# Optimization experiments

Hardware: AMD Instinct MI355X
Metric: run time of the kernel (lower is better)

## Reference

```python
import jax, jax.numpy as jnp
import numpy as np

B, N, T_OBS, N_HEAD = 64, 512, 8, 4
IN_FEAT = T_OBS * 2          # 16
OUT_FEAT = IN_FEAT * 4       # 64 (GAT out / MLP in)
HID1, HID2 = 1024, 512
S, NSAMP = 2, 20
OUT_DIM = S * NSAMP          # 40


def setup_inputs() -> dict:
    key = jax.random.key(0)
    ks = jax.random.split(key, 12)
    x = jax.random.normal(ks[0], (B, N, T_OBS, 2), dtype=jnp.float32)
    # binary adjacency-style mask over the dense node-node attention
    mask = (jax.random.uniform(ks[1], (B, 1, N, N)) > 0.1).astype(jnp.float32)
    xav = lambda k, shp, fi, fo: jax.random.uniform(k, shp, jnp.float32, -1.0, 1.0) * (1.414 * np.sqrt(6.0 / (fi + fo)))
    w = xav(ks[2], (N_HEAD, IN_FEAT, OUT_FEAT), IN_FEAT, OUT_FEAT)
    a_src = xav(ks[3], (N_HEAD, OUT_FEAT, 1), OUT_FEAT, 1)
    a_dst = xav(ks[4], (N_HEAD, OUT_FEAT, 1), OUT_FEAT, 1)
    bias = jnp.zeros((OUT_FEAT,), jnp.float32)
    lin = lambda k, fi, fo: jax.random.uniform(k, (fi, fo), jnp.float32, -1.0, 1.0) * np.sqrt(1.0 / fi)
    W1 = lin(ks[5], OUT_FEAT, HID1); b1 = jnp.zeros((HID1,), jnp.float32)
    W2 = lin(ks[6], HID1, HID2);     b2 = jnp.zeros((HID2,), jnp.float32)
    W3 = lin(ks[7], HID2, OUT_DIM);  b3 = jnp.zeros((OUT_DIM,), jnp.float32)
    return {"x": x, "mask": mask, "w": w, "a_src": a_src, "a_dst": a_dst,
            "bias": bias, "W1": W1, "b1": b1, "W2": W2, "b2": b2, "W3": W3, "b3": b3}


def reference(x, mask, w, a_src, a_dst, bias, W1, b1, W2, b2, W3, b3):
    b, n = x.shape[0], x.shape[1]
    node = x.reshape(b, n, -1)                                   # [B,N,16]
    # per-head projection: [B,N,16] x [H,16,64] -> [B,H,N,64]
    h_prime = jnp.einsum('bni,hio->bhno', node, w)
    attn_src = jnp.einsum('bhno,ho->bhn', h_prime, a_src[..., 0])
    attn_dst = jnp.einsum('bhno,ho->bhn', h_prime, a_dst[..., 0])
    attn = attn_src[..., :, None] * attn_dst[..., None, :]       # [B,H,N,N] outer product
    attn = jnp.where(attn >= 0, attn, 0.2 * attn)                # leaky_relu(0.2)
    attn = jax.nn.softmax(attn, axis=-1)
    # dropout is identity in eval mode
    attn = attn * mask
    out = jnp.einsum('bhnm,bhmo->bno', attn, h_prime) + bias     # sum over heads fused
    out = out + h_prime.sum(axis=1)                              # skip connection
    # MLP: activation BEFORE each linear (as in original MLP.forward)
    y = out
    for W, bb in ((W1, b1), (W2, b2), (W3, b3)):
        y = jax.nn.relu(y) @ W + bb
    y = y.reshape(b, n, NSAMP, -1)[..., 0:S]                     # [B,N,20,2]
    return jnp.clip(jax.nn.sigmoid(y), 0.01, 0.99)
```

## Files before the change

### kernel.cpp

```cpp
#include <hip/hip_runtime.h>
#include <math.h>

typedef short bf16x8 __attribute__((ext_vector_type(8)));
typedef float f32x4 __attribute__((ext_vector_type(4)));

#define BB 64
#define NN 512
#define NH 4
#define FI 16
#define FO 64
#define HD1 1024
#define HD2 512
#define ODIM 40

__device__ __forceinline__ unsigned short f2bf(float f) {
    unsigned u = __float_as_uint(f);
    u += 0x7fffu + ((u >> 16) & 1u);
    return (unsigned short)(u >> 16);
}
__device__ __forceinline__ unsigned pack2(float a, float b) {
    return (unsigned)f2bf(a) | ((unsigned)f2bf(b) << 16);
}
__device__ __forceinline__ void gload16(const void* g, void* l) {
    __builtin_amdgcn_global_load_lds(
        (const __attribute__((address_space(1))) unsigned int*)g,
        (__attribute__((address_space(3))) unsigned int*)l,
        16, 0, 0);
}

__global__ void k_wa(const float* __restrict__ w, const float* __restrict__ a_src,
                     const float* __restrict__ a_dst, float* __restrict__ wa)
{
    int t = threadIdx.x;
    int h = t >> 4;
    float s = 0.f, d = 0.f;
    for (int o = 0; o < FO; ++o) {
        float wv = w[t*FO + o];
        s = fmaf(wv, a_src[h*FO + o], s);
        d = fmaf(wv, a_dst[h*FO + o], d);
    }
    wa[t] = s; wa[64 + t] = d;
}

__global__ __launch_bounds__(256) void k_pack(
    const float* __restrict__ mask, unsigned char* __restrict__ mbits)
{
    __shared__ unsigned char lb[4][64];
    int t = threadIdx.x;
    int r = t >> 6, l = t & 63;
    size_t R = (size_t)blockIdx.x * 4 + r;
    const float4* src = (const float4*)(mask + R*NN + l*8);
    float4 a = src[0], bq = src[1];
    unsigned byte = 0;
    byte |= (a.x  != 0.f) ? 1u   : 0u;
    byte |= (a.y  != 0.f) ? 2u   : 0u;
    byte |= (a.z  != 0.f) ? 4u   : 0u;
    byte |= (a.w  != 0.f) ? 8u   : 0u;
    byte |= (bq.x != 0.f) ? 16u  : 0u;
    byte |= (bq.y != 0.f) ? 32u  : 0u;
    byte |= (bq.z != 0.f) ? 64u  : 0u;
    byte |= (bq.w != 0.f) ? 128u : 0u;
    lb[r][(l & 3)*16 + (l >> 2)] = (unsigned char)byte;
    __syncthreads();
    if (t < 16) {
        int rr = t >> 2, seg = t & 3;
        uint4 v = *(uint4*)&lb[rr][seg*16];
        *(uint4*)&mbits[((size_t)blockIdx.x*4 + rr)*64 + seg*16] = v;
    }
}

__global__ __launch_bounds__(256) void k_proj2(
    const float* __restrict__ x, const float* __restrict__ w,
    const float* __restrict__ bias, const float* __restrict__ wa,
    short* __restrict__ hpT,
    float* __restrict__ asrc, float* __restrict__ adst,
    float* __restrict__ gat)
{
    __shared__ float xS[64][20];
    __shared__ float gS[NH][64][64];
    int b = blockIdx.y;
    int n0 = blockIdx.x * 64;
    int t = threadIdx.x;
    int h = t >> 6, o = t & 63;
    {
        int n = t >> 2, q = t & 3;
        float4 v = *(const float4*)&x[((size_t)b*NN + n0 + n)*FI + q*4];
        *(float4*)&xS[n][q*4] = v;
    }
    float wreg[16];
#pragma unroll
    for (int i = 0; i < FI; ++i) wreg[i] = w[(h*FI + i)*FO + o];
    __syncthreads();

    short* hb = hpT + (size_t)b * (NH*FO*NN);
    for (int nc = 0; nc < 8; ++nc) {
        float acc[8];
#pragma unroll
        for (int k = 0; k < 8; ++k) {
            int n = nc*8 + k;
            float4 a0 = *(const float4*)&xS[n][0];
            float4 a1 = *(const float4*)&xS[n][4];
            float4 a2 = *(const float4*)&xS[n][8];
            float4 a3 = *(const float4*)&xS[n][12];
            float sA = fmaf(a0.x, wreg[0], fmaf(a0.y, wreg[1], fmaf(a0.z, wreg[2], a0.w*wreg[3])));
            float sB = fmaf(a1.x, wreg[4], fmaf(a1.y, wreg[5], fmaf(a1.z, wreg[6], a1.w*wreg[7])));
            float sC = fmaf(a2.x, wreg[8], fmaf(a2.y, wreg[9], fmaf(a2.z, wreg[10], a2.w*wreg[11])));
            float sD = fmaf(a3.x, wreg[12], fmaf(a3.y, wreg[13], fmaf(a3.z, wreg[14], a3.w*wreg[15])));
            float s = (sA + sB) + (sC + sD);
            acc[k] = s;
            gS[h][n][o] = s;
        }
        uint4 p;
        p.x = pack2(acc[0], acc[1]); p.y = pack2(acc[2], acc[3]);
        p.z = pack2(acc[4], acc[5]); p.w = pack2(acc[6], acc[7]);
        int jt = (n0 >> 5) + (nc >> 2);
        *(uint4*)&hb[(size_t)(jt*256 + h*64 + o)*32 + (nc & 3)*8] = p;
    }
    {
        int n = o;
        float vs = 0.f, vd = 0.f;
#pragma unroll
        for (int i = 0; i < FI; ++i) {
            float xv = xS[n][i];
            vs = fmaf(xv, wa[h*FI + i], vs);
            vd = fmaf(xv, wa[64 + h*FI + i], vd);
        }
        asrc[(size_t)(b*NH + h)*NN + n0 + n] = vs;
        adst[(size_t)(b*NH + h)*NN + n0 + n] = vd;
    }
    __syncthreads();
#pragma unroll
    for (int r = 0; r < 16; ++r) {
        int idx = t + r*256;
        int n = idx >> 6, oo = idx & 63;
        float g = bias[oo] + ((gS[0][n][oo] + gS[1][n][oo]) + (gS[2][n][oo] + gS[3][n][oo]));
        gat[((size_t)b*NN + n0 + n)*FO + oo] = g;
    }
}

__global__ __launch_bounds__(512, 2) void k_attn2(
    const short* __restrict__ hpT, const unsigned char* __restrict__ mbits,
    const float* __restrict__ asrc, const float* __restrict__ adst,
    float* __restrict__ gat)
{
    __shared__ float dS[NH*NN];
    __shared__ float dmaxS[NH], dminS[NH];
    __shared__ float part[4*4*64*4];
    int b = blockIdx.y;
    int i0blk = blockIdx.x * 64;
    int t = threadIdx.x;
#pragma unroll
    for (int r = 0; r < 4; ++r) {
        int idx = t + r*512;
        dS[idx] = adst[(size_t)b*(NH*NN) + idx];
    }
    __syncthreads();
    int wave = t >> 6, lane = t & 63;
    int wv4 = wave & 3, hh = (wave >> 2) * 2;
    if (wave < 4) {
        float mx = -INFINITY, mn = INFINITY;
        const float* dh = &dS[wave*NN];
#pragma unroll
        for (int q = 0; q < 8; ++q) {
            float v = dh[lane*8 + q];
            mx = fmaxf(mx, v); mn = fminf(mn, v);
        }
#pragma unroll
        for (int off = 1; off < 64; off <<= 1) {
            mx = fmaxf(mx, __shfl_xor(mx, off));
            mn = fminf(mn, __shfl_xor(mn, off));
        }
        if (lane == 0) { dmaxS[wave] = mx; dminS[wave] = mn; }
    }
    __syncthreads();
    int li = lane & 15, kq = lane >> 4;
    int i = i0blk + wv4*16 + li;
    float s[2], m[2], Ssum[2];
#pragma unroll
    for (int h2 = 0; h2 < 2; ++h2) {
        int h = hh + h2;
        s[h2] = asrc[(size_t)(b*NH + h)*NN + i];
        float dm = s[h2] >= 0.f ? dmaxS[h] : dminS[h];
        float l = s[h2] * dm;
        m[h2] = fmaxf(l, 0.2f*l);
        Ssum[h2] = 0.f;
    }
    f32x4 accH[2][4];
#pragma unroll
    for (int h2 = 0; h2 < 2; ++h2)
#pragma unroll
        for (int ot = 0; ot < 4; ++ot) accH[h2][ot] = (f32x4)0.f;

    unsigned mwarr[4];
    {
        uint4 mv = *(const uint4*)(mbits + ((size_t)(b*NN + i))*64 + kq*16);
        mwarr[0] = mv.x; mwarr[1] = mv.y; mwarr[2] = mv.z; mwarr[3] = mv.w;
    }
    const short* vb = hpT + (size_t)b * (NH*FO*NN);
#pragma unroll
    for (int jt = 0; jt < 16; ++jt) {
        unsigned mbyte = (mwarr[jt >> 2] >> ((jt & 3) * 8)) & 0xffu;
        int j0 = jt*32;
#pragma unroll
        for (int h2 = 0; h2 < 2; ++h2) {
            int h = hh + h2;
            float4 d0 = *(const float4*)&dS[h*NN + j0 + kq*8];
            float4 d1 = *(const float4*)&dS[h*NN + j0 + kq*8 + 4];
            float dv[8] = {d0.x,d0.y,d0.z,d0.w,d1.x,d1.y,d1.z,d1.w};
            float u[8];
#pragma unroll
            for (int q = 0; q < 8; ++q) {
                float v = s[h2]*dv[q];
                v = fmaxf(v, 0.2f*v);
                u[q] = __expf(v - m[h2]);
            }
            Ssum[h2] += ((u[0]+u[1]) + (u[2]+u[3])) + ((u[4]+u[5]) + (u[6]+u[7]));
            float mu[8];
#pragma unroll
            for (int q = 0; q < 8; ++q)
                mu[q] = ((mbyte >> q) & 1u) ? u[q] : 0.f;
            union { bf16x8 v; unsigned uu[4]; } pf;
#pragma unroll
            for (int q = 0; q < 4; ++q)
                pf.uu[q] = pack2(mu[2*q], mu[2*q+1]);
            __builtin_amdgcn_s_setprio(1);
#pragma unroll
            for (int ot = 0; ot < 4; ++ot) {
                bf16x8 vf = *(const bf16x8*)&vb[(size_t)(jt*256 + h*64 + ot*16 + li)*32 + kq*8];
                accH[h2][ot] = __builtin_amdgcn_mfma_f32_16x16x32_bf16(pf.v, vf, accH[h2][ot], 0, 0, 0);
            }
            __builtin_amdgcn_s_setprio(0);
        }
    }
#pragma unroll
    for (int h2 = 0; h2 < 2; ++h2) {
        Ssum[h2] += __shfl_xor(Ssum[h2], 16);
        Ssum[h2] += __shfl_xor(Ssum[h2], 32);
    }
    float rinv[2][4];
#pragma unroll
    for (int h2 = 0; h2 < 2; ++h2)
#pragma unroll
        for (int g = 0; g < 4; ++g)
            rinv[h2][g] = 1.0f / __shfl(Ssum[h2], kq*4 + g);
    f32x4 contrib[4];
#pragma unroll
    for (int ot = 0; ot < 4; ++ot)
#pragma unroll
        for (int g = 0; g < 4; ++g)
            contrib[ot][g] = accH[0][ot][g]*rinv[0][g] + accH[1][ot][g]*rinv[1][g];
    if (wave < 4) {
#pragma unroll
        for (int ot = 0; ot < 4; ++ot) {
            float4 v = {contrib[ot][0], contrib[ot][1], contrib[ot][2], contrib[ot][3]};
            *(float4*)&part[((wv4*4 + ot)*64 + lane)*4] = v;
        }
    }
    __syncthreads();
    if (wave >= 4) {
#pragma unroll
        for (int ot = 0; ot < 4; ++ot) {
            float4 p = *(const float4*)&part[((wv4*4 + ot)*64 + lane)*4];
#pragma unroll
            for (int g = 0; g < 4; ++g) {
                int ii = i0blk + wv4*16 + kq*4 + g;
                int oo = ot*16 + li;
                size_t ix = ((size_t)b*NN + ii)*FO + oo;
                float pg = (g == 0) ? p.x : (g == 1) ? p.y : (g == 2) ? p.z : p.w;
                gat[ix] += contrib[ot][g] + pg;
            }
        }
    }
}

__global__ __launch_bounds__(256) void k_conv(
    const float* __restrict__ W1, const float* __restrict__ W2, const float* __restrict__ W3,
    short* __restrict__ w1t, short* __restrict__ w2f, short* __restrict__ w3t)
{
    int idx = blockIdx.x * 256 + threadIdx.x;
    if (idx < HD1*FO) {
        int n = idx >> 6, k = idx & 63;
        w1t[idx] = (short)f2bf(W1[k*HD1 + n]);
    } else if (idx < HD1*FO + HD2*HD1) {
        int i2 = idx - HD1*FO;
        int e = i2 & 7, kqq = (i2 >> 3) & 3, n = (i2 >> 5) & 511, ks = i2 >> 14;
        int k = ks*32 + kqq*8 + e;
        w2f[i2] = (short)f2bf(W2[k*HD2 + n]);
    } else if (idx < HD1*FO + HD2*HD1 + 48*HD2) {
        int i3 = idx - (HD1*FO + HD2*HD1);
        int n = i3 >> 9, k = i3 & 511;
        w3t[i3] = (short)(n < ODIM ? f2bf(W3[k*ODIM + n]) : 0);
    }
}

__global__ __launch_bounds__(256, 2) void k_mlpA(
    const float* __restrict__ gat,
    const short* __restrict__ w1t, const float* __restrict__ b1,
    short* __restrict__ h1g)
{
    __shared__ char a0b[8192];
    int t = threadIdx.x;
    int lane = t & 63, wave = t >> 6;
    int li = lane & 15, kq = lane >> 4;
    int m0 = blockIdx.x * 64;

    {
        int row = t >> 2, c0 = (t & 3) * 16;
        const float4* g = (const float4*)&gat[(size_t)(m0 + row) * FO + c0];
        float4 v0 = g[0], v1 = g[1], v2 = g[2], v3 = g[3];
        uint4 p0, p1;
        p0.x = pack2(fmaxf(v0.x,0.f), fmaxf(v0.y,0.f));
        p0.y = pack2(fmaxf(v0.z,0.f), fmaxf(v0.w,0.f));
        p0.z = pack2(fmaxf(v1.x,0.f), fmaxf(v1.y,0.f));
        p0.w = pack2(fmaxf(v1.z,0.f), fmaxf(v1.w,0.f));
        p1.x = pack2(fmaxf(v2.x,0.f), fmaxf(v2.y,0.f));
        p1.y = pack2(fmaxf(v2.z,0.f), fmaxf(v2.w,0.f));
        p1.z = pack2(fmaxf(v3.x,0.f), fmaxf(v3.y,0.f));
        p1.w = pack2(fmaxf(v3.z,0.f), fmaxf(v3.w,0.f));
        int base = row*128 + c0*2;
        *(uint4*)(a0b + (base ^ ((row&7)<<4)))      = p0;
        *(uint4*)(a0b + ((base+16) ^ ((row&7)<<4))) = p1;
    }
    __syncthreads();

    for (int c = 0; c < 4; ++c) {
        int n0 = wave * 256 + c * 64;
        f32x4 acc[4][4];
#pragma unroll
        for (int mt = 0; mt < 4; ++mt)
#pragma unroll
            for (int nt = 0; nt < 4; ++nt) acc[mt][nt] = (f32x4)0.f;
#pragma unroll
        for (int ks = 0; ks < 2; ++ks) {
            int k0 = ks * 32;
            bf16x8 xf[4];
#pragma unroll
            for (int mt = 0; mt < 4; ++mt) {
                int row = mt * 16 + li;
                int addr = (row * 128 + k0 * 2 + kq * 16) ^ ((row & 7) << 4);
                xf[mt] = *(bf16x8*)(a0b + addr);
            }
#pragma unroll
            for (int nt = 0; nt < 4; ++nt) {
                int col = n0 + nt * 16 + li;
                bf16x8 wf = *(const bf16x8*)(w1t + col * 64 + k0 + kq * 8);
#pragma unroll
                for (int mt = 0; mt < 4; ++mt)
                    acc[mt][nt] = __builtin_amdgcn_mfma_f32_16x16x32_bf16(wf, xf[mt], acc[mt][nt], 0, 0, 0);
            }
        }
#pragma unroll
        for (int mt = 0; mt < 4; ++mt)
#pragma unroll
            for (int nt = 0; nt < 4; ++nt) {
                int m = mt * 16 + li;
                int nb = n0 + nt * 16 + kq * 4;
                float4 bb = *(const float4*)&b1[nb];
                float v0 = fmaxf(acc[mt][nt][0] + bb.x, 0.f);
                float v1 = fmaxf(acc[mt][nt][1] + bb.y, 0.f);
                float v2 = fmaxf(acc[mt][nt][2] + bb.z, 0.f);
                float v3 = fmaxf(acc[mt][nt][3] + bb.w, 0.f);
                uint2 pw; pw.x = pack2(v0, v1); pw.y = pack2(v2, v3);
                *(uint2*)&h1g[(size_t)(m0 + m) * HD1 + nb] = pw;
            }
    }
}

__global__ __launch_bounds__(512, 2) void k_mlpB(
    const short* __restrict__ h1g,
    const short* __restrict__ w2f, const float* __restrict__ b2,
    const short* __restrict__ w3t, const float* __restrict__ b3,
    float* __restrict__ out)
{
    extern __shared__ char smem[];
    int t = threadIdx.x;
    int lane = t & 63, wave = t >> 6;
    int li = lane & 15, kq = lane >> 4;
    int m0 = blockIdx.x * 128;

    auto STAGE = [&](int i, int ks) {
        char* base = smem + i * 8192;
        int row = wave * 16 + (lane >> 2);
        int slotS = (lane & 3) ^ ((row >> 1) & 3);
        const short* src = h1g + (size_t)(m0 + row) * HD1 + ks * 32 + slotS * 8;
        gload16(src, base + wave * 1024);
    };
    const short* wfbase = w2f + ((size_t)(wave*64 + li)*4 + kq)*8;

    f32x4 acc2[8][4];
#pragma unroll
    for (int mt = 0; mt < 8; ++mt)
#pragma unroll
        for (int nt = 0; nt < 4; ++nt) acc2[mt][nt] = (f32x4)0.f;

    bf16x8 wf0[4], wf1[4];
    __builtin_amdgcn_sched_barrier(0);
    STAGE(0, 0);
#pragma unroll
    for (int nt = 0; nt < 4; ++nt) wf0[nt] = *(const bf16x8*)(wfbase + 0*16384 + nt*512);
    __builtin_amdgcn_sched_barrier(0);
    STAGE(1, 1);
#pragma unroll
    for (int nt = 0; nt < 4; ++nt) wf1[nt] = *(const bf16x8*)(wfbase + 1*16384 + nt*512);
    __builtin_amdgcn_sched_barrier(0);

    for (int ks = 0; ks < 32; ++ks) {
        int cur = ks & 1;
        if (ks < 31) { asm volatile("s_waitcnt vmcnt(5)" ::: "memory"); }
        else         { asm volatile("s_waitcnt vmcnt(0)" ::: "memory"); }
        __builtin_amdgcn_sched_barrier(0);
        __builtin_amdgcn_s_barrier();
        __builtin_amdgcn_sched_barrier(0);

        char* base = smem + cur * 8192;
        bf16x8 xf[8];
#pragma unroll
        for (int mt = 0; mt < 8; ++mt) {
            int m = mt * 16 + li;
            int slot = kq ^ ((m >> 1) & 3);
            xf[mt] = *(bf16x8*)(base + m * 64 + slot * 16);
        }
        asm volatile("s_waitcnt lgkmcnt(0)" ::: "memory");
        __builtin_amdgcn_sched_barrier(0);
        __builtin_amdgcn_s_barrier();
        __builtin_amdgcn_sched_barrier(0);

        bf16x8 wfn[4];
        if (ks < 30) {
            STAGE(cur, ks + 2);
#pragma unroll
            for (int nt = 0; nt < 4; ++nt)
                wfn[nt] = *(const bf16x8*)(wfbase + (size_t)(ks+2)*16384 + nt*512);
        }
        __builtin_amdgcn_sched_barrier(0);

        __builtin_amdgcn_s_setprio(1);
#pragma unroll
        for (int nt = 0; nt < 4; ++nt)
#pragma unroll
            for (int mt = 0; mt < 8; ++mt)
                acc2[mt][nt] = __builtin_amdgcn_mfma_f32_16x16x32_bf16(wf0[nt], xf[mt], acc2[mt][nt], 0, 0, 0);
        __builtin_amdgcn_s_setprio(0);
        if (ks < 30) {
#pragma unroll
            for (int nt = 0; nt < 4; ++nt) { wf0[nt] = wf1[nt]; wf1[nt] = wfn[nt]; }
        } else {
#pragma unroll
            for (int nt = 0; nt < 4; ++nt) wf0[nt] = wf1[nt];
        }
    }
    __syncthreads();

#pragma unroll
    for (int mt = 0; mt < 8; ++mt)
#pragma unroll
        for (int nt = 0; nt < 4; ++nt) {
            int m = mt * 16 + li;
            int nb = wave * 64 + nt * 16 + kq * 4;
            float4 bb = *(const float4*)&b2[nb];
            float v0 = fmaxf(acc2[mt][nt][0] + bb.x, 0.f);
            float v1 = fmaxf(acc2[mt][nt][1] + bb.y, 0.f);
            float v2 = fmaxf(acc2[mt][nt][2] + bb.z, 0.f);
            float v3 = fmaxf(acc2[mt][nt][3] + bb.w, 0.f);
            uint2 pw; pw.x = pack2(v0, v1); pw.y = pack2(v2, v3);
            int addr = (m * 1024 + nb * 2) ^ ((m & 7) << 4);
            *(uint2*)(smem + addr) = pw;
        }
    __syncthreads();

    f32x4 acc3[3];
#pragma unroll
    for (int nt = 0; nt < 3; ++nt) acc3[nt] = (f32x4)0.f;
#pragma unroll
    for (int ks = 0; ks < 16; ++ks) {
        int k0 = ks * 32;
        int m = wave * 16 + li;
        int addr = (m * 1024 + k0 * 2 + kq * 16) ^ ((m & 7) << 4);
        bf16x8 xfr = *(bf16x8*)(smem + addr);
#pragma unroll
        for (int nt = 0; nt < 3; ++nt) {
            int col = nt * 16 + li;
            bf16x8 wfr = *(const bf16x8*)(w3t + col * 512 + k0 + kq * 8);
            acc3[nt] = __builtin_amdgcn_mfma_f32_16x16x32_bf16(wfr, xfr, acc3[nt], 0, 0, 0);
        }
    }
#pragma unroll
    for (int nt = 0; nt < 3; ++nt)
#pragma unroll
        for (int g = 0; g < 4; ++g) {
            int n = nt * 16 + kq * 4 + g;
            if (n < ODIM) {
                int m = wave * 16 + li;
                float s = acc3[nt][g] + b3[n];
                s = 1.f / (1.f + __expf(-s));
                s = fminf(fmaxf(s, 0.01f), 0.99f);
                out[(size_t)(m0 + m) * ODIM + n] = s;
            }
        }
}

extern "C" void kernel_launch(void* const* d_in, const int* in_sizes, int n_in,
                              void* d_out, int out_size, void* d_ws, size_t ws_size,
                              hipStream_t stream)
{
    const float* x     = (const float*)d_in[0];
    const float* mask  = (const float*)d_in[1];
    const float* w     = (const float*)d_in[2];
    const float* a_src = (const float*)d_in[3];
    const float* a_dst = (const float*)d_in[4];
    const float* bias  = (const float*)d_in[5];
    const float* W1    = (const float*)d_in[6];
    const float* b1    = (const float*)d_in[7];
    const float* W2    = (const float*)d_in[8];
    const float* b2    = (const float*)d_in[9];
    const float* W3    = (const float*)d_in[10];
    const float* b3    = (const float*)d_in[11];
    float* out = (float*)d_out;

    char* p = (char*)d_ws;
    short* h1g = (short*)p;
    short* hpT = (short*)p;  p += (size_t)BB*NH*FO*NN*2;
    float* asrc = (float*)p; p += (size_t)BB*NH*NN*4;
    float* adst = (float*)p; p += (size_t)BB*NH*NN*4;
    p = (char*)d_ws + (size_t)BB*NN*HD1*2;
    float* gat  = (float*)p; p += (size_t)BB*NN*FO*4;
    short* w1t  = (short*)p; p += (size_t)HD1*FO*2;
    short* w2f  = (short*)p; p += (size_t)HD2*HD1*2;
    short* w3t  = (short*)p; p += (size_t)48*HD2*2;
    float* wa   = (float*)p; p += 128*4;
    unsigned char* mbits = (unsigned char*)p; p += (size_t)BB*NN*64;

    k_wa   <<<1, 64, 0, stream>>>(w, a_src, a_dst, wa);
    k_pack <<<BB*NN/4, 256, 0, stream>>>(mask, mbits);
    k_conv <<<(HD1*FO + HD2*HD1 + 48*HD2)/256, 256, 0, stream>>>(W1, W2, W3, w1t, w2f, w3t);
    k_proj2<<<dim3(NN/64, BB), 256, 0, stream>>>(x, w, bias, wa, hpT, asrc, adst, gat);
    k_attn2<<<dim3(NN/64, BB), 512, 0, stream>>>(hpT, mbits, asrc, adst, gat);
    k_mlpA <<<BB*NN/64, 256, 0, stream>>>(gat, w1t, b1, h1g);
    k_mlpB <<<BB*NN/128, 512, 131072, stream>>>(h1g, w2f, b2, w3t, b3, out);
}
```

Baseline: 160.4 us.

## Fuse first MLP layer into second-layer kernel, producing h1 tiles in LDS

Measured after the change: 156.9 us. -2.2%, faster.

```diff
diff --git a/kernel.cpp b/kernel.cpp
--- a/kernel.cpp
+++ b/kernel.cpp
@@ -20,12 +20,6 @@
 }
 __device__ __forceinline__ unsigned pack2(float a, float b) {
     return (unsigned)f2bf(a) | ((unsigned)f2bf(b) << 16);
-}
-__device__ __forceinline__ void gload16(const void* g, void* l) {
-    __builtin_amdgcn_global_load_lds(
-        (const __attribute__((address_space(1))) unsigned int*)g,
-        (__attribute__((address_space(3))) unsigned int*)l,
-        16, 0, 0);
 }
 
 __global__ void k_wa(const float* __restrict__ w, const float* __restrict__ a_src,
@@ -293,16 +287,20 @@
     }
 }
 
-__global__ __launch_bounds__(256, 2) void k_mlpA(
+__global__ __launch_bounds__(512, 2) void k_mlpB(
     const float* __restrict__ gat,
     const short* __restrict__ w1t, const float* __restrict__ b1,
-    short* __restrict__ h1g)
-{
-    __shared__ char a0b[8192];
+    const short* __restrict__ w2f, const float* __restrict__ b2,
+    const short* __restrict__ w3t, const float* __restrict__ b3,
+    float* __restrict__ out)
+{
+    extern __shared__ char smem[];
+    char* a0b = smem;
+    char* h1s = smem + 16384;
     int t = threadIdx.x;
     int lane = t & 63, wave = t >> 6;
     int li = lane & 15, kq = lane >> 4;
-    int m0 = blockIdx.x * 64;
+    int m0 = blockIdx.x * 128;
 
     {
         int row = t >> 2, c0 = (t & 3) * 16;
@@ -323,68 +321,38 @@
     }
     __syncthreads();
 
-    for (int c = 0; c < 4; ++c) {
-        int n0 = wave * 256 + c * 64;
-        f32x4 acc[4][4];
-#pragma unroll
-        for (int mt = 0; mt < 4; ++mt)
-#pragma unroll
-            for (int nt = 0; nt < 4; ++nt) acc[mt][nt] = (f32x4)0.f;
-#pragma unroll
-        for (int ks = 0; ks < 2; ++ks) {
-            int k0 = ks * 32;
-            bf16x8 xf[4];
-#pragma unroll
-            for (int mt = 0; mt < 4; ++mt) {
-                int row = mt * 16 + li;
-                int addr = (row * 128 + k0 * 2 + kq * 16) ^ ((row & 7) << 4);
-                xf[mt] = *(bf16x8*)(a0b + addr);
-            }
-#pragma unroll
-            for (int nt = 0; nt < 4; ++nt) {
-                int col = n0 + nt * 16 + li;
-                bf16x8 wf = *(const bf16x8*)(w1t + col * 64 + k0 + kq * 8);
-#pragma unroll
-                for (int mt = 0; mt < 4; ++mt)
-                    acc[mt][nt] = __builtin_amdgcn_mfma_f32_16x16x32_bf16(wf, xf[mt], acc[mt][nt], 0, 0, 0);
-            }
-        }
-#pragma unroll
-        for (int mt = 0; mt < 4; ++mt)
-#pragma unroll
-            for (int nt = 0; nt < 4; ++nt) {
-                int m = mt * 16 + li;
-                int nb = n0 + nt * 16 + kq * 4;
-                float4 bb = *(const float4*)&b1[nb];
-                float v0 = fmaxf(acc[mt][nt][0] + bb.x, 0.f);
-                float v1 = fmaxf(acc[mt][nt][1] + bb.y, 0.f);
-                float v2 = fmaxf(acc[mt][nt][2] + bb.z, 0.f);
-                float v3 = fmaxf(acc[mt][nt][3] + bb.w, 0.f);
-                uint2 pw; pw.x = pack2(v0, v1); pw.y = pack2(v2, v3);
-                *(uint2*)&h1g[(size_t)(m0 + m) * HD1 + nb] = pw;
-            }
-    }
-}
-
-__global__ __launch_bounds__(512, 2) void k_mlpB(
-    const short* __restrict__ h1g,
-    const short* __restrict__ w2f, const float* __restrict__ b2,
-    const short* __restrict__ w3t, const float* __restrict__ b3,
-    float* __restrict__ out)
-{
-    extern __shared__ char smem[];
-    int t = threadIdx.x;
-    int lane = t & 63, wave = t >> 6;
-    int li = lane & 15, kq = lane >> 4;
-    int m0 = blockIdx.x * 128;
-
-    auto STAGE = [&](int i, int ks) {
-        char* base = smem + i * 8192;
-        int row = wave * 16 + (lane >> 2);
-        int slotS = (lane & 3) ^ ((row >> 1) & 3);
-        const short* src = h1g + (size_t)(m0 + row) * HD1 + ks * 32 + slotS * 8;
-        gload16(src, base + wave * 1024);
+    bf16x8 a0f[2];
+#pragma unroll
+    for (int k0s = 0; k0s < 2; ++k0s) {
+        int row = wave*16 + li;
+        int addr = (row*128 + k0s*64 + kq*16) ^ ((row&7)<<4);
+        a0f[k0s] = *(bf16x8*)(a0b + addr);
+    }
+
+    auto PRODUCE = [&](int bufi, int ks) {
+        char* hb = h1s + bufi*8192;
+#pragma unroll
+        for (int klt = 0; klt < 2; ++klt) {
+            int n = ks*32 + klt*16 + li;
+            bf16x8 w1f0 = *(const bf16x8*)(w1t + n*64 + kq*8);
+            bf16x8 w1f1 = *(const bf16x8*)(w1t + n*64 + 32 + kq*8);
+            f32x4 ah = (f32x4)0.f;
+            ah = __builtin_amdgcn_mfma_f32_16x16x32_bf16(w1f0, a0f[0], ah, 0, 0, 0);
+            ah = __builtin_amdgcn_mfma_f32_16x16x32_bf16(w1f1, a0f[1], ah, 0, 0, 0);
+            int m = wave*16 + li;
+            int nb = ks*32 + klt*16 + kq*4;
+            float4 bb = *(const float4*)&b1[nb];
+            float v0 = fmaxf(ah[0] + bb.x, 0.f);
+            float v1 = fmaxf(ah[1] + bb.y, 0.f);
+            float v2 = fmaxf(ah[2] + bb.z, 0.f);
+            float v3 = fmaxf(ah[3] + bb.w, 0.f);
+            uint2 pw; pw.x = pack2(v0, v1); pw.y = pack2(v2, v3);
+            int s0 = klt*2 + (kq >> 1);
+            int p = s0 ^ ((m >> 1) & 3);
+            *(uint2*)(hb + m*64 + p*16 + (kq & 1)*8) = pw;
+        }
     };
+
     const short* wfbase = w2f + ((size_t)(wave*64 + li)*4 + kq)*8;
 
     f32x4 acc2[8][4];
@@ -393,61 +361,53 @@
 #pragma unroll
         for (int nt = 0; nt < 4; ++nt) acc2[mt][nt] = (f32x4)0.f;
 
-    bf16x8 wf0[4], wf1[4];
+    PRODUCE(0, 0);
+    asm volatile("s_waitcnt lgkmcnt(0)" ::: "memory");
     __builtin_amdgcn_sched_barrier(0);
-    STAGE(0, 0);
-#pragma unroll
-    for (int nt = 0; nt < 4; ++nt) wf0[nt] = *(const bf16x8*)(wfbase + 0*16384 + nt*512);
-    __builtin_amdgcn_sched_barrier(0);
-    STAGE(1, 1);
-#pragma unroll
-    for (int nt = 0; nt < 4; ++nt) wf1[nt] = *(const bf16x8*)(wfbase + 1*16384 + nt*512);
+    __builtin_amdgcn_s_barrier();
     __builtin_amdgcn_sched_barrier(0);
 
     for (int ks = 0; ks < 32; ++ks) {
         int cur = ks & 1;
-        if (ks < 31) { asm volatile("s_waitcnt vmcnt(5)" ::: "memory"); }
-        else         { asm volatile("s_waitcnt vmcnt(0)" ::: "memory"); }
+        bf16x8 wf[4];
+#pragma unroll
+        for (int nt = 0; nt < 4; ++nt)
+            wf[nt] = *(const bf16x8*)(wfbase + (size_t)ks*16384 + nt*512);
+        char* base = h1s + cur*8192;
+        bf16x8 xfa[4];
+#pragma unroll
+        for (int mt = 0; mt < 4; ++mt) {
+            int m = mt * 16 + li;
+            int slot = kq ^ ((m >> 1) & 3);
+            xfa[mt] = *(bf16x8*)(base + m * 64 + slot * 16);
+        }
+        if (ks < 31) PRODUCE(cur ^ 1, ks + 1);
+        asm volatile("s_waitcnt lgkmcnt(0)" ::: "memory");
+        __builtin_amdgcn_sched_barrier(0);
+        __builtin_amdgcn_s_setprio(1);
+#pragma unroll
+        for (int nt = 0; nt < 4; ++nt)
+#pragma unroll
+            for (int mt = 0; mt < 4; ++mt)
+                acc2[mt][nt] = __builtin_amdgcn_mfma_f32_16x16x32_bf16(wf[nt], xfa[mt], acc2[mt][nt], 0, 0, 0);
+        bf16x8 xfb[4];
+#pragma unroll
+        for (int mt = 0; mt < 4; ++mt) {
+            int m = (mt + 4) * 16 + li;
+            int slot = kq ^ ((m >> 1) & 3);
+            xfb[mt] = *(bf16x8*)(base + m * 64 + slot * 16);
+        }
+        asm volatile("s_waitcnt lgkmcnt(0)" ::: "memory");
+        __builtin_amdgcn_sched_barrier(0);
+#pragma unroll
+        for (int nt = 0; nt < 4; ++nt)
+#pragma unroll
+            for (int mt = 0; mt < 4; ++mt)
+                acc2[mt+4][nt] = __builtin_amdgcn_mfma_f32_16x16x32_bf16(wf[nt], xfb[mt], acc2[mt+4][nt], 0, 0, 0);
+        __builtin_amdgcn_s_setprio(0);
         __builtin_amdgcn_sched_barrier(0);
         __builtin_amdgcn_s_barrier();
         __builtin_amdgcn_sched_barrier(0);
-
-        char* base = smem + cur * 8192;
-        bf16x8 xf[8];
-#pragma unroll
-        for (int mt = 0; mt < 8; ++mt) {
-            int m = mt * 16 + li;
-            int slot = kq ^ ((m >> 1) & 3);
-            xf[mt] = *(bf16x8*)(base + m * 64 + slot * 16);
-        }
-        asm volatile("s_waitcnt lgkmcnt(0)" ::: "memory");
-        __builtin_amdgcn_sched_barrier(0);
-        __builtin_amdgcn_s_barrier();
-        __builtin_amdgcn_sched_barrier(0);
-
-        bf16x8 wfn[4];
-        if (ks < 30) {
-            STAGE(cur, ks + 2);
-#pragma unroll
-            for (int nt = 0; nt < 4; ++nt)
-                wfn[nt] = *(const bf16x8*)(wfbase + (size_t)(ks+2)*16384 + nt*512);
-        }
-        __builtin_amdgcn_sched_barrier(0);
-
-        __builtin_amdgcn_s_setprio(1);
-#pragma unroll
-        for (int nt = 0; nt < 4; ++nt)
-#pragma unroll
-            for (int mt = 0; mt < 8; ++mt)
-                acc2[mt][nt] = __builtin_amdgcn_mfma_f32_16x16x32_bf16(wf0[nt], xf[mt], acc2[mt][nt], 0, 0, 0);
-        __builtin_amdgcn_s_setprio(0);
-        if (ks < 30) {
-#pragma unroll
-            for (int nt = 0; nt < 4; ++nt) { wf0[nt] = wf1[nt]; wf1[nt] = wfn[nt]; }
-        } else {
-#pragma unroll
-            for (int nt = 0; nt < 4; ++nt) wf0[nt] = wf1[nt];
-        }
     }
     __syncthreads();
 
@@ -518,11 +478,9 @@
     float* out = (float*)d_out;
 
     char* p = (char*)d_ws;
-    short* h1g = (short*)p;
     short* hpT = (short*)p;  p += (size_t)BB*NH*FO*NN*2;
     float* asrc = (float*)p; p += (size_t)BB*NH*NN*4;
     float* adst = (float*)p; p += (size_t)BB*NH*NN*4;
-    p = (char*)d_ws + (size_t)BB*NN*HD1*2;
     float* gat  = (float*)p; p += (size_t)BB*NN*FO*4;
     short* w1t  = (short*)p; p += (size_t)HD1*FO*2;
     short* w2f  = (short*)p; p += (size_t)HD2*HD1*2;
@@ -535,6 +493,5 @@
     k_conv <<<(HD1*FO + HD2*HD1 + 48*HD2)/256, 256, 0, stream>>>(W1, W2, W3, w1t, w2f, w3t);
     k_proj2<<<dim3(NN/64, BB), 256, 0, stream>>>(x, w, bias, wa, hpT, asrc, adst, gat);
     k_attn2<<<dim3(NN/64, BB), 512, 0, stream>>>(hpT, mbits, asrc, adst, gat);
-    k_mlpA <<<BB*NN/64, 256, 0, stream>>>(gat, w1t, b1, h1g);
-    k_mlpB <<<BB*NN/128, 512, 131072, stream>>>(h1g, w2f, b2, w3t, b3, out);
-}
+    k_mlpB <<<BB*NN/128, 512, 131072, stream>>>(gat, w1t, b1, w2f, b2, w3t, b3, out);
+}
```
